# Performance work log

Measured on AMD Instinct MI355X. Metric: run time of the kernel, lower is better.

The kernel has to match this reference:

```python
import jax, jax.numpy as jnp
import numpy as np

# Module constants derived from default grid_config
D = 59          # depth bins: (60-1)/1
C_OUT = 64
X, Y, Z = 128, 128, 7
STRIDE = 16
GRID_LB = np.array([-51.2, -51.2, -2.5], dtype=np.float32)
GRID_IV = np.array([0.8, 0.8, 1.0], dtype=np.float32)
D0, DSTEP = 1.0, 1.0

B, N, C_IN, H, W = 4, 6, 256, 16, 44


def _voxel_coords():
    xs, ys, zs = np.meshgrid(np.arange(X), np.arange(Y), np.arange(Z), indexing='ij')
    coords = np.stack([xs, ys, zs], axis=-1).reshape(-1, 3).astype(np.float32)
    coords = coords * GRID_IV + GRID_LB  # [V, 3] ego-frame voxel centers
    return coords


def _camera_rig(rng):
    """Realistic 6-camera rig: yawed cameras looking outward, z_cam = forward."""
    c2e = np.zeros((B, N, 4, 4), dtype=np.float32)
    K = np.zeros((B, N, 3, 3), dtype=np.float32)
    for b in range(B):
        for n in range(N):
            a = 2.0 * np.pi * n / N + 0.02 * rng.standard_normal()
            f = np.array([np.cos(a), np.sin(a), 0.0])           # camera forward (z_cam)
            x_cam = np.array([-np.sin(a), np.cos(a), 0.0])      # camera right
            y_cam = np.array([0.0, 0.0, -1.0])                   # camera down
            R = np.stack([x_cam, y_cam, f], axis=1)              # columns = cam axes in ego
            t = 1.0 * f + np.array([0.0, 0.0, 1.5])
            c2e[b, n, :3, :3] = R
            c2e[b, n, :3, 3] = t
            c2e[b, n, 3, 3] = 1.0
            fl = 400.0 + 5.0 * rng.standard_normal()
            K[b, n] = np.array([[fl, 0.0, 352.0], [0.0, fl, 128.0], [0.0, 0.0, 1.0]])
    return c2e, K


def setup_inputs() -> dict:
    key = jax.random.key(0)
    k1, k2, k3 = jax.random.split(key, 3)
    img_feats = jax.random.normal(k1, (B, N, C_IN, H, W), dtype=jnp.float32)
    c2e, K = _camera_rig(np.random.default_rng(0))
    # depth_net: 1x1 conv in_channels -> D + C_OUT
    w_depth = jax.random.normal(k2, (D + C_OUT, C_IN), dtype=jnp.float32) * (1.0 / np.sqrt(C_IN))
    b_depth = jax.random.normal(k3, (D + C_OUT,), dtype=jnp.float32) * 0.01
    return {
        'img_feats': img_feats,
        'cam2ego': jnp.asarray(c2e),
        'cam_intrinsics': jnp.asarray(K),
        'w_depth': w_depth,
        'b_depth': b_depth,
    }


def reference(img_feats, cam2ego, cam_intrinsics, w_depth, b_depth):
    Bc, Nc, C, Hc, Wc = img_feats.shape
    # 1x1 conv == per-pixel linear
    x = jnp.einsum('bnchw,oc->bnhwo', img_feats, w_depth) + b_depth  # [B,N,H,W,D+C_OUT]
    depth = jax.nn.softmax(x[..., :D], axis=-1)                      # [B,N,H,W,D]
    feat = x[..., D:]                                                # [B,N,H,W,C_OUT]

    vox = jnp.asarray(_voxel_coords())                               # [V,3]
    V = vox.shape[0]
    vox_h = jnp.concatenate([vox, jnp.ones((V, 1), vox.dtype)], axis=1)  # [V,4]

    e2c = jnp.linalg.inv(cam2ego)                                    # [B,N,4,4]
    cam = jnp.einsum('bnij,vj->bnvi', e2c, vox_h)[..., :3]           # [B,N,V,3]
    z = cam[..., 2]
    z_safe = jnp.maximum(z, 0.1)
    norm = cam[..., :2] / z_safe[..., None]
    homo = jnp.concatenate([norm, jnp.ones_like(z[..., None])], axis=-1)  # [B,N,V,3]
    img = jnp.einsum('bnij,bnvj->bnvi', cam_intrinsics, homo)[..., :2]
    fc = img / STRIDE                                                # feature-plane coords

    depth_bin = ((z - D0) / DSTEP).astype(jnp.int32)                 # trunc toward 0, matches .long()
    valid = (
        (fc[..., 0] >= 0) & (fc[..., 0] < Wc)
        & (fc[..., 1] >= 0) & (fc[..., 1] < Hc)
        & (z > 0.5)
        & (depth_bin >= 0) & (depth_bin < D)
    )

    u = jnp.clip(fc[..., 0].astype(jnp.int32), 0, Wc - 1)            # [B,N,V]
    v = jnp.clip(fc[..., 1].astype(jnp.int32), 0, Hc - 1)
    d = jnp.clip(depth_bin, 0, D - 1)
    hw = v * Wc + u

    feat_flat = feat.reshape(Bc, Nc, Hc * Wc, C_OUT)
    sampled_feat = jnp.take_along_axis(feat_flat, hw[..., None], axis=2)   # [B,N,V,C_OUT]
    depth_flat = depth.reshape(Bc, Nc, Hc * Wc * D)
    sampled_depth = jnp.take_along_axis(depth_flat, hw * D + d, axis=2)    # [B,N,V]

    wgt = sampled_depth * valid.astype(sampled_depth.dtype)
    # scatter_add at flat_idx == voxel index (identity) -> masked sum over cameras
    bev = jnp.einsum('bnv,bnvc->bvc', wgt, sampled_feat)             # [B,V,C_OUT]
    bev = bev.reshape(Bc, X, Y, Z, C_OUT).sum(axis=3)                # collapse Z
    bev = bev.transpose(0, 3, 2, 1)                                  # [B,C_OUT,Y,X]
    return bev, depth
```

## Files before the change

kernel.cpp:

```cpp
#include <hip/hip_runtime.h>
#include <math.h>

#define D_BINS 59
#define CO     64
#define CI     256
#define NB     4
#define NC     6
#define H_IMG  16
#define W_IMG  44
#define HW     704
#define NPIX   (NB*NC*HW)
#define XD     128
#define YD     128
#define ZD     7
#define NOUT   123
#define PXT    32
#define XW     132

typedef float v2f __attribute__((ext_vector_type(2)));

__device__ void inv_rigid(const float* __restrict__ M, float* __restrict__ o) {
    double a = M[0], b = M[1], c = M[2], t0 = M[3];
    double d = M[4], e = M[5], f = M[6], t1 = M[7];
    double g = M[8], h = M[9], ii = M[10], t2 = M[11];
    double A00 = e*ii - f*h, A01 = c*h - b*ii, A02 = b*f - c*e;
    double A10 = f*g - d*ii, A11 = a*ii - c*g, A12 = c*d - a*f;
    double A20 = d*h - e*g,  A21 = b*g - a*h,  A22 = a*e - b*d;
    double det = a*A00 + b*A10 + c*A20;
    double inv = 1.0 / det;
    double r00 = A00*inv, r01 = A01*inv, r02 = A02*inv;
    double r10 = A10*inv, r11 = A11*inv, r12 = A12*inv;
    double r20 = A20*inv, r21 = A21*inv, r22 = A22*inv;
    o[0] = (float)r00; o[1] = (float)r01; o[2]  = (float)r02;
    o[3] = (float)(-(r00*t0 + r01*t1 + r02*t2));
    o[4] = (float)r10; o[5] = (float)r11; o[6]  = (float)r12;
    o[7] = (float)(-(r10*t0 + r11*t1 + r12*t2));
    o[8] = (float)r20; o[9] = (float)r21; o[10] = (float)r22;
    o[11] = (float)(-(r20*t0 + r21*t1 + r22*t2));
}

__global__ __launch_bounds__(256) void k_pre(
    const float* __restrict__ wd, const float* __restrict__ c2e,
    float* __restrict__ wt2, float* __restrict__ e2c) {
    const int o = blockIdx.x;
    const int k = threadIdx.x;
    float v = (o < NOUT) ? wd[(size_t)o * CI + k] : 0.f;
    wt2[(size_t)(k >> 1) * 256 + o * 2 + (k & 1)] = v;
    if (blockIdx.x == 0 && k < NB * NC)
        inv_rigid(c2e + k * 16, e2c + k * 12);
}

__global__ __launch_bounds__(256) void k_head(
    const float* __restrict__ img, const float* __restrict__ wt2,
    const float* __restrict__ bd, float* __restrict__ depth_out,
    float* __restrict__ feat_ws) {
    __shared__ float A[128 * 64];
    __shared__ float Xs[PXT * XW];
    __shared__ float S[PXT];

    const int tid = threadIdx.x;
    const int wv  = tid >> 6;
    const int ln  = tid & 63;
    const int p0  = blockIdx.x * PXT;
    const int pw0 = (wv & 1) << 4;
    const int kh  = wv >> 1;
    const int kb  = __builtin_amdgcn_readfirstlane(kh << 6);

    const int bn  = p0 / HW;
    const int hw0 = p0 - bn * HW;
    const float* gsrc = img + (size_t)bn * CI * HW + hw0;
#pragma unroll 8
    for (int it = 0; it < 32; ++it) {
        int idx = tid + it * 256;
        int ch = idx >> 5, px = idx & 31;
        A[(ch >> 1) * 64 + px * 2 + (ch & 1)] = gsrc[ch * HW + px];
    }
    __syncthreads();

    v2f accA[16], accB[16];
#pragma unroll
    for (int p = 0; p < 16; ++p) { accA[p] = (v2f)(0.f); accB[p] = (v2f)(0.f); }

#pragma unroll 2
    for (int k2i = 0; k2i < 64; ++k2i) {
        const int k2 = kb + k2i;
        float4 w4 = *(const float4*)(wt2 + (size_t)k2 * 256 + ln * 4);
        v2f wA = {w4.x, w4.y};
        v2f wB = {w4.z, w4.w};
        const float* ar = A + k2 * 64 + pw0 * 2;
#pragma unroll
        for (int i = 0; i < 8; ++i) {
            float4 aq = *(const float4*)(ar + i * 4);
            v2f a0 = {aq.x, aq.y};
            v2f a1 = {aq.z, aq.w};
            accA[2*i]   = __builtin_elementwise_fma(a0, wA, accA[2*i]);
            accB[2*i]   = __builtin_elementwise_fma(a0, wB, accB[2*i]);
            accA[2*i+1] = __builtin_elementwise_fma(a1, wA, accA[2*i+1]);
            accB[2*i+1] = __builtin_elementwise_fma(a1, wB, accB[2*i+1]);
        }
    }

    if (kh == 0) {
#pragma unroll
        for (int p = 0; p < 16; ++p) {
            v2f v = { accA[p].x + accA[p].y, accB[p].x + accB[p].y };
            *(v2f*)(Xs + (pw0 + p) * XW + 2 * ln) = v;
        }
    }
    __syncthreads();
    if (kh == 1) {
        float b0 = (2 * ln     < NOUT) ? bd[2 * ln]     : 0.f;
        float b1 = (2 * ln + 1 < NOUT) ? bd[2 * ln + 1] : 0.f;
#pragma unroll
        for (int p = 0; p < 16; ++p) {
            v2f s = *(const v2f*)(Xs + (pw0 + p) * XW + 2 * ln);
            v2f v = { (s.x + (accA[p].x + accA[p].y)) + b0,
                      (s.y + (accB[p].x + accB[p].y)) + b1 };
            *(v2f*)(Xs + (pw0 + p) * XW + 2 * ln) = v;
        }
    }
    __syncthreads();

    for (int g = tid; g < PXT * CO; g += 256) {
        int p = g >> 6, c = g & 63;
        feat_ws[(size_t)(p0 + p) * CO + c] = Xs[p * XW + 59 + c];
    }
    if (tid < PXT) {
        float* row = Xs + tid * XW;
        float m = row[0];
        for (int o = 1; o < D_BINS; ++o) m = fmaxf(m, row[o]);
        float s = 0.f;
        for (int o = 0; o < D_BINS; ++o) {
            float e = __expf(row[o] - m);
            row[o] = e;
            s += e;
        }
        S[tid] = 1.f / s;
    }
    __syncthreads();
    for (int g = tid; g < PXT * D_BINS; g += 256) {
        int p = g / D_BINS;
        int o = g - p * D_BINS;
        depth_out[(size_t)p0 * D_BINS + g] = Xs[p * XW + o] * S[p];
    }
}

__global__ __launch_bounds__(256) void k_splat(
    const float* __restrict__ e2c, const float* __restrict__ Kmat,
    const float* __restrict__ depth_g, const float* __restrict__ feat_ws,
    float* __restrict__ bev) {
    __shared__ int   hw_s[ZD][64];
    __shared__ float wgt_s[ZD][64];

    const int tx = threadIdx.x;
    const int cq = threadIdx.y;
    const int x = blockIdx.x * 64 + tx;
    const int y = blockIdx.y;
    const int b = blockIdx.z;
    const float wx = (float)x * 0.8f + (-51.2f);
    const float wy = (float)y * 0.8f + (-51.2f);

    float acc[16];
#pragma unroll
    for (int m = 0; m < 16; ++m) acc[m] = 0.f;

    for (int n = 0; n < NC; ++n) {
        const int bn = b * NC + n;
        const float* E = e2c + bn * 12;
        const float* Km = Kmat + bn * 9;
        const float k00 = Km[0], k01 = Km[1], k02 = Km[2];
        const float k10 = Km[3], k11 = Km[4], k12 = Km[5];
        const float e02 = E[2], e12 = E[6], e22 = E[10];
        const float bx0 = E[0] * wx + E[1] * wy + E[3];
        const float bx1 = E[4] * wx + E[5] * wy + E[7];
        const float bx2 = E[8] * wx + E[9] * wy + E[11];

#pragma unroll
        for (int zz = 0; zz < 2; ++zz) {
            const int z = cq + zz * 4;
            if (z < ZD) {
                const float wz = -2.5f + (float)z;
                const float cx = bx0 + e02 * wz;
                const float cy = bx1 + e12 * wz;
                const float cz = bx2 + e22 * wz;
                const float zs = fmaxf(cz, 0.1f);
                const float rz = 1.0f / zs;
                const float xn = cx * rz;
                const float yn = cy * rz;
                const float fu = (k00 * xn + k01 * yn + k02) * 0.0625f;
                const float fv = (k10 * xn + k11 * yn + k12) * 0.0625f;
                const int bin = (int)(cz - 1.0f);
                const bool valid = (fu >= 0.f) & (fu < (float)W_IMG) &
                                   (fv >= 0.f) & (fv < (float)H_IMG) &
                                   (cz > 0.5f) & (bin >= 0) & (bin < D_BINS);
                int hw = -1;
                float wgt = 0.f;
                if (valid) {
                    int u = (int)fu;
                    int v = (int)fv;
                    hw = v * W_IMG + u;
                    wgt = depth_g[((size_t)bn * HW + hw) * D_BINS + bin];
                }
                hw_s[z][tx] = hw;
                wgt_s[z][tx] = wgt;
            }
        }
        __syncthreads();

#pragma unroll
        for (int z = 0; z < ZD; ++z) {
            const int hw = hw_s[z][tx];
            if (hw >= 0) {
                const float wgt = wgt_s[z][tx];
                const float4* fp =
                    (const float4*)(feat_ws + ((size_t)bn * HW + hw) * CO + cq * 16);
                float4 f0 = fp[0], f1 = fp[1], f2 = fp[2], f3 = fp[3];
                acc[0]  = fmaf(wgt, f0.x, acc[0]);
                acc[1]  = fmaf(wgt, f0.y, acc[1]);
                acc[2]  = fmaf(wgt, f0.z, acc[2]);
                acc[3]  = fmaf(wgt, f0.w, acc[3]);
                acc[4]  = fmaf(wgt, f1.x, acc[4]);
                acc[5]  = fmaf(wgt, f1.y, acc[5]);
                acc[6]  = fmaf(wgt, f1.z, acc[6]);
                acc[7]  = fmaf(wgt, f1.w, acc[7]);
                acc[8]  = fmaf(wgt, f2.x, acc[8]);
                acc[9]  = fmaf(wgt, f2.y, acc[9]);
                acc[10] = fmaf(wgt, f2.z, acc[10]);
                acc[11] = fmaf(wgt, f2.w, acc[11]);
                acc[12] = fmaf(wgt, f3.x, acc[12]);
                acc[13] = fmaf(wgt, f3.y, acc[13]);
                acc[14] = fmaf(wgt, f3.z, acc[14]);
                acc[15] = fmaf(wgt, f3.w, acc[15]);
            }
        }
        __syncthreads();
    }
    float* ob = bev + (((size_t)b * CO + cq * 16) * YD + y) * XD + x;
#pragma unroll
    for (int m = 0; m < 16; ++m) ob[(size_t)m * YD * XD] = acc[m];
}

extern "C" void kernel_launch(void* const* d_in, const int* in_sizes, int n_in,
                              void* d_out, int out_size, void* d_ws, size_t ws_size,
                              hipStream_t stream) {
    const float* img  = (const float*)d_in[0];
    const float* c2e  = (const float*)d_in[1];
    const float* Kmat = (const float*)d_in[2];
    const float* wd   = (const float*)d_in[3];
    const float* bd   = (const float*)d_in[4];
    float* bev = (float*)d_out;
    float* depth_out = bev + (size_t)NB * CO * YD * XD;
    float* feat_ws = (float*)d_ws;
    float* wt2 = feat_ws + (size_t)NPIX * CO;
    float* e2c = wt2 + 128 * 256;

    k_pre<<<128, 256, 0, stream>>>(wd, c2e, wt2, e2c);
    k_head<<<528, 256, 0, stream>>>(img, wt2, bd, depth_out, feat_ws);
    k_splat<<<dim3(2, YD, NB), dim3(64, 4, 1), 0, stream>>>(e2c, Kmat, depth_out,
                                                            feat_ws, bev);
}
```

Baseline: 125.0 us.

## Restructure depth head GEMM: per-lane pixels with register inputs, split outputs across blocks

The 1x1-conv head kernel no longer stages the input tile in shared memory. Each lane now owns one pixel and loads its 256 input channels into registers in chunks of 64. Each wave computes 16 output-channel pairs, and a second grid dimension splits the 123 outputs into two halves of 64. The block tile grows to 64 pixels, and the split-K reduction through shared memory is gone. Weights are read straight from global memory as uniform loads, which likely become broadcast scalar loads. The cost is that image inputs are read twice (once per output half) and register pressure rises from the 64-float array.

```diff
diff --git a/kernel.cpp b/kernel.cpp
--- a/kernel.cpp
+++ b/kernel.cpp
@@ -14,8 +14,9 @@
 #define YD     128
 #define ZD     7
 #define NOUT   123
-#define PXT    32
-#define XW     132
+#define PXT    64
+#define NTILE  264
+#define XW     66
 
 typedef float v2f __attribute__((ext_vector_type(2)));
 
@@ -54,7 +55,6 @@
     const float* __restrict__ img, const float* __restrict__ wt2,
     const float* __restrict__ bd, float* __restrict__ depth_out,
     float* __restrict__ feat_ws) {
-    __shared__ float A[128 * 64];
     __shared__ float Xs[PXT * XW];
     __shared__ float S[PXT];
 
@@ -62,86 +62,70 @@
     const int wv  = tid >> 6;
     const int ln  = tid & 63;
     const int p0  = blockIdx.x * PXT;
-    const int pw0 = (wv & 1) << 4;
-    const int kh  = wv >> 1;
-    const int kb  = __builtin_amdgcn_readfirstlane(kh << 6);
+    const int ob  = (int)blockIdx.y << 6;
+    const int o0  = __builtin_amdgcn_readfirstlane(ob + (wv << 4));
 
     const int bn  = p0 / HW;
     const int hw0 = p0 - bn * HW;
-    const float* gsrc = img + (size_t)bn * CI * HW + hw0;
-#pragma unroll 8
-    for (int it = 0; it < 32; ++it) {
-        int idx = tid + it * 256;
-        int ch = idx >> 5, px = idx & 31;
-        A[(ch >> 1) * 64 + px * 2 + (ch & 1)] = gsrc[ch * HW + px];
+    const float* base = img + (size_t)bn * CI * HW + hw0 + ln;
+
+    v2f acc[16];
+#pragma unroll
+    for (int j = 0; j < 16; ++j) acc[j] = (v2f)(0.f);
+
+    float a[64];
+    for (int kc = 0; kc < 4; ++kc) {
+#pragma unroll
+        for (int c = 0; c < 64; ++c)
+            a[c] = base[(size_t)(kc * 64 + c) * HW];
+#pragma unroll
+        for (int k2 = 0; k2 < 32; ++k2) {
+            v2f av = { a[2 * k2], a[2 * k2 + 1] };
+            const v2f* w =
+                (const v2f*)(wt2 + (size_t)(kc * 32 + k2) * 256) + o0;
+#pragma unroll
+            for (int j = 0; j < 16; ++j)
+                acc[j] = __builtin_elementwise_fma(av, w[j], acc[j]);
+        }
+    }
+
+#pragma unroll
+    for (int j = 0; j < 16; ++j) {
+        int o = o0 + j;
+        if (o < NOUT)
+            Xs[ln * XW + (o - ob)] = (acc[j].x + acc[j].y) + bd[o];
     }
     __syncthreads();
 
-    v2f accA[16], accB[16];
-#pragma unroll
-    for (int p = 0; p < 16; ++p) { accA[p] = (v2f)(0.f); accB[p] = (v2f)(0.f); }
-
-#pragma unroll 2
-    for (int k2i = 0; k2i < 64; ++k2i) {
-        const int k2 = kb + k2i;
-        float4 w4 = *(const float4*)(wt2 + (size_t)k2 * 256 + ln * 4);
-        v2f wA = {w4.x, w4.y};
-        v2f wB = {w4.z, w4.w};
-        const float* ar = A + k2 * 64 + pw0 * 2;
-#pragma unroll
-        for (int i = 0; i < 8; ++i) {
-            float4 aq = *(const float4*)(ar + i * 4);
-            v2f a0 = {aq.x, aq.y};
-            v2f a1 = {aq.z, aq.w};
-            accA[2*i]   = __builtin_elementwise_fma(a0, wA, accA[2*i]);
-            accB[2*i]   = __builtin_elementwise_fma(a0, wB, accB[2*i]);
-            accA[2*i+1] = __builtin_elementwise_fma(a1, wA, accA[2*i+1]);
-            accB[2*i+1] = __builtin_elementwise_fma(a1, wB, accB[2*i+1]);
-        }
-    }
-
-    if (kh == 0) {
-#pragma unroll
-        for (int p = 0; p < 16; ++p) {
-            v2f v = { accA[p].x + accA[p].y, accB[p].x + accB[p].y };
-            *(v2f*)(Xs + (pw0 + p) * XW + 2 * ln) = v;
-        }
-    }
-    __syncthreads();
-    if (kh == 1) {
-        float b0 = (2 * ln     < NOUT) ? bd[2 * ln]     : 0.f;
-        float b1 = (2 * ln + 1 < NOUT) ? bd[2 * ln + 1] : 0.f;
-#pragma unroll
-        for (int p = 0; p < 16; ++p) {
-            v2f s = *(const v2f*)(Xs + (pw0 + p) * XW + 2 * ln);
-            v2f v = { (s.x + (accA[p].x + accA[p].y)) + b0,
-                      (s.y + (accB[p].x + accB[p].y)) + b1 };
-            *(v2f*)(Xs + (pw0 + p) * XW + 2 * ln) = v;
-        }
-    }
-    __syncthreads();
-
-    for (int g = tid; g < PXT * CO; g += 256) {
-        int p = g >> 6, c = g & 63;
-        feat_ws[(size_t)(p0 + p) * CO + c] = Xs[p * XW + 59 + c];
-    }
-    if (tid < PXT) {
-        float* row = Xs + tid * XW;
-        float m = row[0];
-        for (int o = 1; o < D_BINS; ++o) m = fmaxf(m, row[o]);
-        float s = 0.f;
-        for (int o = 0; o < D_BINS; ++o) {
-            float e = __expf(row[o] - m);
-            row[o] = e;
-            s += e;
-        }
-        S[tid] = 1.f / s;
-    }
-    __syncthreads();
-    for (int g = tid; g < PXT * D_BINS; g += 256) {
-        int p = g / D_BINS;
-        int o = g - p * D_BINS;
-        depth_out[(size_t)p0 * D_BINS + g] = Xs[p * XW + o] * S[p];
+    if (blockIdx.y == 0) {
+        for (int g = tid; g < PXT * 5; g += 256) {
+            int p = g / 5, c = g - p * 5;
+            feat_ws[(size_t)(p0 + p) * CO + c] = Xs[p * XW + 59 + c];
+        }
+        if (tid < PXT) {
+            float* row = Xs + tid * XW;
+            float m = row[0];
+            for (int o = 1; o < D_BINS; ++o) m = fmaxf(m, row[o]);
+            float s = 0.f;
+            for (int o = 0; o < D_BINS; ++o) {
+                float e = __expf(row[o] - m);
+                row[o] = e;
+                s += e;
+            }
+            S[tid] = 1.f / s;
+        }
+        __syncthreads();
+        for (int g = tid; g < PXT * D_BINS; g += 256) {
+            int p = g / D_BINS;
+            int o = g - p * D_BINS;
+            depth_out[(size_t)p0 * D_BINS + g] = Xs[p * XW + o] * S[p];
+        }
+    } else {
+        for (int g = tid; g < PXT * D_BINS; g += 256) {
+            int p = g / D_BINS;
+            int col = g - p * D_BINS;
+            feat_ws[(size_t)(p0 + p) * CO + 5 + col] = Xs[p * XW + col];
+        }
     }
 }
 
@@ -255,7 +239,7 @@
     float* e2c = wt2 + 128 * 256;
 
     k_pre<<<128, 256, 0, stream>>>(wd, c2e, wt2, e2c);
-    k_head<<<528, 256, 0, stream>>>(img, wt2, bd, depth_out, feat_ws);
+    k_head<<<dim3(NTILE, 2), 256, 0, stream>>>(img, wt2, bd, depth_out, feat_ws);
     k_splat<<<dim3(2, YD, NB), dim3(64, 4, 1), 0, stream>>>(e2c, Kmat, depth_out,
                                                             feat_ws, bev);
 }
```

Measured after the change: 126.2 us. No clear change (+0.9%).
